# Kernel tuning notes

Measured on AMD Instinct MI355X. Metric: run time of the kernel, lower is better.

## Reference

```python
import jax, jax.numpy as jnp
import numpy as np


def fps(xyz, npoint):
    # Farthest point sampling. xyz: [B, N, 3] -> idx [B, npoint] int32
    B, N, _ = xyz.shape
    d0 = jnp.full((B, N), 1e10, xyz.dtype)
    far0 = jnp.zeros((B,), jnp.int32)

    def step(carry, _):
        dist, far = carry
        centroid = jnp.take_along_axis(xyz, far[:, None, None], axis=1)  # [B,1,3]
        d = jnp.sum((xyz - centroid) ** 2, axis=-1)                      # [B,N]
        dist = jnp.minimum(dist, d)
        nxt = jnp.argmax(dist, axis=-1).astype(jnp.int32)
        return (dist, nxt), far

    _, idx = jax.lax.scan(step, (d0, far0), None, length=npoint)
    return idx.T  # [B, npoint]


def ball_query(radius, nsample, xyz, new_xyz):
    # xyz [B,N,3], new_xyz [B,S,3] -> idx [B,S,nsample] int32
    N = xyz.shape[1]
    sqr = (jnp.sum(new_xyz ** 2, -1)[:, :, None]
           + jnp.sum(xyz ** 2, -1)[:, None, :]
           - 2.0 * jnp.einsum('bsd,bnd->bsn', new_xyz, xyz))  # [B,S,N]
    idx = jnp.broadcast_to(jnp.arange(N, dtype=jnp.int32), sqr.shape)
    idx = jnp.where(sqr > radius * radius, N, idx)
    idx = jnp.sort(idx, axis=-1)[..., :nsample]
    first = idx[..., :1]  # centers are in xyz, so at least one in-radius index exists
    return jnp.where(idx == N, first, idx)


def _gather(x, idx):
    # x [B,N,C], idx [B,S,K] -> [B,S,K,C]
    return jax.vmap(lambda xb, ib: xb[ib])(x, idx)


def set_abstraction(xyz, points, npoint, radius, nsample, layers):
    # xyz [B,N,3]; points [B,N,D] or None; layers: list of (W [Co,Ci], b [Co])
    fps_idx = fps(xyz, npoint)                                   # [B,S]
    new_xyz = jnp.take_along_axis(xyz, fps_idx[..., None], axis=1)  # [B,S,3]
    idx = ball_query(radius, nsample, xyz, new_xyz)              # [B,S,K]
    grouped = _gather(xyz, idx) - new_xyz[:, :, None, :]         # [B,S,K,3] centered
    if points is not None:
        grouped = jnp.concatenate([grouped, _gather(points, idx)], axis=-1)
    feats = grouped  # [B,S,K,Cin]
    for W, b in layers:  # shared 1x1 conv MLP (BN folded, eval mode) + ReLU
        feats = jax.nn.relu(jnp.einsum('bskc,oc->bsko', feats, W) + b)
    new_points = jnp.max(feats, axis=2)  # max-pool over neighborhood -> [B,S,Cout]
    return new_xyz, new_points.transpose(0, 2, 1)  # [B,S,3], [B,Cout,S]


def setup_inputs() -> dict:
    key = jax.random.key(0)
    ks = jax.random.split(key, 13)
    xyz = jax.random.uniform(ks[0], (8, 6, 32768), dtype=jnp.float32)
    dims1 = [(64, 6), (64, 64), (128, 64)]
    dims2 = [(128, 131), (128, 128), (285, 128)]
    inp = {'xyz': xyz}
    i = 1
    for pre, dims in (('sa1', dims1), ('sa2', dims2)):
        for j, (o, c) in enumerate(dims, 1):
            inp[f'{pre}_w{j}'] = jax.random.normal(ks[i], (o, c), jnp.float32) * (1.0 / np.sqrt(c))
            inp[f'{pre}_b{j}'] = jax.random.normal(ks[i + 6], (o,), jnp.float32) * 0.05
            i += 1
    return inp


def reference(xyz, sa1_w1, sa1_b1, sa1_w2, sa1_b2, sa1_w3, sa1_b3,
              sa2_w1, sa2_b1, sa2_w2, sa2_b2, sa2_w3, sa2_b3):
    norm = xyz[:, 3:, :].transpose(0, 2, 1)   # [B,N,3]
    xyz3 = xyz[:, :3, :].transpose(0, 2, 1)   # [B,N,3]
    l1_xyz, l1_points = set_abstraction(
        xyz3, norm, 512, 0.025, 32,
        [(sa1_w1, sa1_b1), (sa1_w2, sa1_b2), (sa1_w3, sa1_b3)])
    l2_xyz, l2_points = set_abstraction(
        l1_xyz, l1_points.transpose(0, 2, 1), 256, 0.05, 64,
        [(sa2_w1, sa2_b1), (sa2_w2, sa2_b2), (sa2_w3, sa2_b3)])
    return l2_xyz.transpose(0, 2, 1), l2_points.transpose(0, 2, 1)  # [B,3,256],[B,256,285]
```

## Files before the change

kernel.cpp:

```cpp
#include <hip/hip_runtime.h>

#define N1 32768
#define NP1 512
#define NS1 32
#define N2 512
#define NP2 256
#define NS2 64

__device__ __forceinline__ float fadd(float a, float b){ return __fadd_rn(a,b); }
__device__ __forceinline__ float fmul(float a, float b){ return __fmul_rn(a,b); }
__device__ __forceinline__ float fsub(float a, float b){ return __fsub_rn(a,b); }

__device__ __forceinline__ float dist3(float px,float py,float pz,float cx,float cy,float cz){
    float dx = fsub(px,cx), dy = fsub(py,cy), dz = fsub(pz,cz);
    return fadd(fadd(fmul(dx,dx), fmul(dy,dy)), fmul(dz,dz));
}
__device__ __forceinline__ float sumsq3(float x,float y,float z){
    return fadd(fadd(fmul(x,x), fmul(y,y)), fmul(z,z));
}
__device__ __forceinline__ float dot3(float ax,float ay,float az,float bx,float by,float bz){
    return fadd(fadd(fmul(ax,bx), fmul(ay,by)), fmul(az,bz));
}

__device__ __forceinline__ unsigned long long shflmax64(unsigned long long k, int off){
    unsigned long long o = __shfl_xor(k, off, 64);
    return o > k ? o : k;
}

#define FPS1_M  16
#define FPS1_TB 256

__global__ __launch_bounds__(FPS1_TB) void fps1_kernel(const float* __restrict__ xyz,
                                                       float* __restrict__ new_xyz1,
                                                       unsigned long long* __restrict__ bests)
{
    const int m = blockIdx.x;
    const int b = blockIdx.y;
    const int t = threadIdx.x;
    const int lane = t & 63;
    const int wid  = t >> 6;
    const int slot = m*4 + wid;
    const float* xb = xyz + (size_t)b * 6 * N1;

    const int base = m * (N1 / FPS1_M);
    float px[8], py[8], pz[8], dd[8];
#pragma unroll
    for (int j = 0; j < 8; ++j) {
        int n = base + t + j * FPS1_TB;
        px[j] = xb[n];
        py[j] = xb[N1 + n];
        pz[j] = xb[2*N1 + n];
        dd[j] = 1e10f;
    }

    float cx = xb[0], cy = xb[N1], cz = xb[2*N1];

    for (int s = 0; s < NP1; ++s) {
        if (m == 0 && t == 0) {
            float* o = new_xyz1 + ((size_t)b*NP1 + s)*3;
            o[0] = cx; o[1] = cy; o[2] = cz;
        }
        if (s == NP1 - 1) break;

        float bv = -1.0f; int bi = base + t;
#pragma unroll
        for (int j = 0; j < 8; ++j) {
            float d  = dist3(px[j],py[j],pz[j],cx,cy,cz);
            float nd = fminf(dd[j], d);
            dd[j] = nd;
            if (nd > bv) { bv = nd; bi = base + t + j*FPS1_TB; }
        }
        unsigned long long pk = ((unsigned long long)__float_as_uint(bv) << 15)
                              | (unsigned long long)(32767 - bi);
        pk = shflmax64(pk, 1);  pk = shflmax64(pk, 2);  pk = shflmax64(pk, 4);
        pk = shflmax64(pk, 8);  pk = shflmax64(pk, 16); pk = shflmax64(pk, 32);

        unsigned long long* slotPar = bests + ((size_t)b*2 + (s & 1))*64;
        if (lane == 0)
            __hip_atomic_store(slotPar + slot, (pk << 10) | (unsigned long long)s,
                               __ATOMIC_RELAXED, __HIP_MEMORY_SCOPE_AGENT);

        unsigned long long myv = 0; bool done = false;
        float ccx = 0.f, ccy = 0.f, ccz = 0.f;
        while (__ballot(done) != 0xFFFFFFFFFFFFFFFFull) {
            if (!done) {
                unsigned long long v = __hip_atomic_load(slotPar + lane,
                                         __ATOMIC_RELAXED, __HIP_MEMORY_SCOPE_AGENT);
                if ((unsigned)(v & 1023ull) == (unsigned)s) {
                    done = true; myv = v;
                    int idx = 32767 - (int)((v >> 10) & 0x7fffull);
                    ccx = xb[idx]; ccy = xb[N1 + idx]; ccz = xb[2*N1 + idx];
                }
            }
        }
        unsigned long long w = myv;
        w = shflmax64(w, 1);  w = shflmax64(w, 2);  w = shflmax64(w, 4);
        w = shflmax64(w, 8);  w = shflmax64(w, 16); w = shflmax64(w, 32);
        int wl = (int)__ffsll(__ballot(myv == w)) - 1;
        cx = __shfl(ccx, wl, 64);
        cy = __shfl(ccy, wl, 64);
        cz = __shfl(ccz, wl, 64);
    }
}

__global__ __launch_bounds__(64) void fps2_kernel(const float* __restrict__ new_xyz1,
                                                  float* __restrict__ new_xyz2,
                                                  float* __restrict__ out0)
{
    const int b = blockIdx.x;
    const int t = threadIdx.x;
    __shared__ float c3[N2*3];
    const float* src = new_xyz1 + (size_t)b*N2*3;
    for (int e = t; e < N2*3; e += 64) c3[e] = src[e];
    __syncthreads();

    float px[8], py[8], pz[8], dd[8];
#pragma unroll
    for (int j = 0; j < 8; ++j) {
        int n = t + j*64;
        px[j] = c3[n*3]; py[j] = c3[n*3+1]; pz[j] = c3[n*3+2];
        dd[j] = 1e10f;
    }
    int cur = 0;
    for (int s = 0; s < NP2; ++s) {
        float cx = c3[cur*3], cy = c3[cur*3+1], cz = c3[cur*3+2];
        if (t == 0) {
            float* o = new_xyz2 + ((size_t)b*NP2 + s)*3;
            o[0]=cx; o[1]=cy; o[2]=cz;
            out0[b*3*NP2 + s]         = cx;
            out0[b*3*NP2 + NP2 + s]   = cy;
            out0[b*3*NP2 + 2*NP2 + s] = cz;
        }
        float bv = -1.0f; int bi = 0;
#pragma unroll
        for (int j = 0; j < 8; ++j) {
            float d  = dist3(px[j],py[j],pz[j],cx,cy,cz);
            float nd = fminf(dd[j], d);
            dd[j] = nd;
            int n = t + j*64;
            if (nd > bv) { bv = nd; bi = n; }
        }
        unsigned long long pk = ((unsigned long long)__float_as_uint(bv) << 9)
                              | (unsigned long long)(511 - bi);
        pk = shflmax64(pk, 1);  pk = shflmax64(pk, 2);  pk = shflmax64(pk, 4);
        pk = shflmax64(pk, 8);  pk = shflmax64(pk, 16); pk = shflmax64(pk, 32);
        cur = 511 - (int)(pk & 511ull);
    }
}

__global__ __launch_bounds__(64) void ball1_kernel(const float* __restrict__ xyz,
                                                   const float* __restrict__ new_xyz1,
                                                   int* __restrict__ idx1, float r2)
{
    const int s = blockIdx.x, b = blockIdx.y;
    const int lane = threadIdx.x;
    const float* xb = xyz + (size_t)b*6*N1;
    const float* cp = new_xyz1 + ((size_t)b*NP1 + s)*3;
    float cx = cp[0], cy = cp[1], cz = cp[2];
    float snew = sumsq3(cx,cy,cz);
    int* out = idx1 + ((size_t)b*NP1 + s)*NS1;
    int cnt = 0, first = 0;
    for (int ch = 0; ch < N1/64; ++ch) {
        int n = ch*64 + lane;
        float x = xb[n], y = xb[N1+n], z = xb[2*N1+n];
        float sx  = sumsq3(x,y,z);
        float dt  = dot3(cx,cy,cz,x,y,z);
        float sqr = fsub(fadd(snew, sx), fmul(2.0f, dt));
        bool inb = !(sqr > r2);
        unsigned long long mask = __ballot(inb);
        if (mask) {
            if (cnt == 0) first = ch*64 + (int)(__ffsll((unsigned long long)mask) - 1);
            if (inb) {
                int pos = cnt + (int)__popcll(mask & ((1ull << lane) - 1ull));
                if (pos < NS1) out[pos] = n;
            }
            cnt += (int)__popcll(mask);
            if (cnt >= NS1) break;
        }
    }
    int c = cnt < NS1 ? cnt : NS1;
    if (lane < NS1 && lane >= c) out[lane] = first;
}

__global__ __launch_bounds__(64) void ball2_kernel(const float* __restrict__ new_xyz1,
                                                   const float* __restrict__ new_xyz2,
                                                   int* __restrict__ idx2, float r2)
{
    const int s = blockIdx.x, b = blockIdx.y;
    const int lane = threadIdx.x;
    const float* pb = new_xyz1 + (size_t)b*N2*3;
    const float* cp = new_xyz2 + ((size_t)b*NP2 + s)*3;
    float cx = cp[0], cy = cp[1], cz = cp[2];
    float snew = sumsq3(cx,cy,cz);
    int* out = idx2 + ((size_t)b*NP2 + s)*NS2;
    int cnt = 0, first = 0;
    for (int ch = 0; ch < N2/64; ++ch) {
        int n = ch*64 + lane;
        float x = pb[n*3], y = pb[n*3+1], z = pb[n*3+2];
        float sx  = sumsq3(x,y,z);
        float dt  = dot3(cx,cy,cz,x,y,z);
        float sqr = fsub(fadd(snew, sx), fmul(2.0f, dt));
        bool inb = !(sqr > r2);
        unsigned long long mask = __ballot(inb);
        if (mask) {
            if (cnt == 0) first = ch*64 + (int)(__ffsll((unsigned long long)mask) - 1);
            if (inb) {
                int pos = cnt + (int)__popcll(mask & ((1ull << lane) - 1ull));
                if (pos < NS2) out[pos] = n;
            }
            cnt += (int)__popcll(mask);
            if (cnt >= NS2) break;
        }
    }
    int c = cnt < NS2 ? cnt : NS2;
    if (lane >= c) out[lane] = first;
}

__global__ __launch_bounds__(256) void mlp1_kernel(const float* __restrict__ xyz,
    const float* __restrict__ new_xyz1, const int* __restrict__ idx1,
    const float* __restrict__ W1, const float* __restrict__ B1,
    const float* __restrict__ W2, const float* __restrict__ B2,
    const float* __restrict__ W3, const float* __restrict__ B3,
    float* __restrict__ l1_points)
{
    const int s = blockIdx.x, b = blockIdx.y;
    const int t = threadIdx.x;
    const float* xb = xyz + (size_t)b*6*N1;
    __shared__ __align__(16) float inb_[NS1][6];
    __shared__ __align__(16) float h1_[NS1][64];
    __shared__ __align__(16) float h2_[NS1][64];
    __shared__ __align__(16) float red_[2][128];
    __shared__ int sidx[NS1];

    const float* cp = new_xyz1 + ((size_t)b*NP1 + s)*3;
    float c0 = cp[0], c1 = cp[1], c2 = cp[2];
    if (t < NS1) sidx[t] = idx1[((size_t)b*NP1+s)*NS1 + t];
    __syncthreads();
    if (t < NS1*6) {
        int k = t / 6, c = t % 6;
        int n = sidx[k];
        float v = xb[(size_t)c*N1 + n];
        if (c == 0) v -= c0; else if (c == 1) v -= c1; else if (c == 2) v -= c2;
        inb_[k][c] = v;
    }
    __syncthreads();
    {
        int o = t & 63, kg = t >> 6;
        float w[6];
#pragma unroll
        for (int c = 0; c < 6; ++c) w[c] = W1[o*6+c];
        float bias = B1[o];
#pragma unroll
        for (int kk = 0; kk < 8; ++kk) {
            int k = kg*8 + kk;
            float a = 0.f;
#pragma unroll
            for (int c = 0; c < 6; ++c) a = fmaf(inb_[k][c], w[c], a);
            h1_[k][o] = fmaxf(a + bias, 0.f);
        }
    }
    __syncthreads();
    {
        int o = t & 63, kg = t >> 6;
        float acc[8] = {};
        for (int ch = 0; ch < 8; ++ch) {
            const float4 wa = *(const float4*)&W2[o*64 + ch*8];
            const float4 wbv = *(const float4*)&W2[o*64 + ch*8 + 4];
#pragma unroll
            for (int kk = 0; kk < 8; ++kk) {
                int k = kg*8+kk;
                const float4 a0 = *(const float4*)&h1_[k][ch*8];
                const float4 a1 = *(const float4*)&h1_[k][ch*8+4];
                acc[kk] = fmaf(a0.x, wa.x, acc[kk]);
                acc[kk] = fmaf(a0.y, wa.y, acc[kk]);
                acc[kk] = fmaf(a0.z, wa.z, acc[kk]);
                acc[kk] = fmaf(a0.w, wa.w, acc[kk]);
                acc[kk] = fmaf(a1.x, wbv.x, acc[kk]);
                acc[kk] = fmaf(a1.y, wbv.y, acc[kk]);
                acc[kk] = fmaf(a1.z, wbv.z, acc[kk]);
                acc[kk] = fmaf(a1.w, wbv.w, acc[kk]);
            }
        }
        float bias = B2[o];
#pragma unroll
        for (int kk = 0; kk < 8; ++kk) h2_[kg*8+kk][o] = fmaxf(acc[kk] + bias, 0.f);
    }
    __syncthreads();
    {
        int o = t & 127, kg = t >> 7;
        float acc[16] = {};
        for (int ch = 0; ch < 8; ++ch) {
            const float4 wa = *(const float4*)&W3[o*64 + ch*8];
            const float4 wbv = *(const float4*)&W3[o*64 + ch*8 + 4];
#pragma unroll
            for (int kk = 0; kk < 16; ++kk) {
                int k = kg*16+kk;
                const float4 a0 = *(const float4*)&h2_[k][ch*8];
                const float4 a1 = *(const float4*)&h2_[k][ch*8+4];
                acc[kk] = fmaf(a0.x, wa.x, acc[kk]);
                acc[kk] = fmaf(a0.y, wa.y, acc[kk]);
                acc[kk] = fmaf(a0.z, wa.z, acc[kk]);
                acc[kk] = fmaf(a0.w, wa.w, acc[kk]);
                acc[kk] = fmaf(a1.x, wbv.x, acc[kk]);
                acc[kk] = fmaf(a1.y, wbv.y, acc[kk]);
                acc[kk] = fmaf(a1.z, wbv.z, acc[kk]);
                acc[kk] = fmaf(a1.w, wbv.w, acc[kk]);
            }
        }
        float bias = B3[o];
        float m = -1e30f;
#pragma unroll
        for (int kk = 0; kk < 16; ++kk) m = fmaxf(m, fmaxf(acc[kk] + bias, 0.f));
        red_[kg][o] = m;
    }
    __syncthreads();
    if (t < 128) {
        float m = fmaxf(red_[0][t], red_[1][t]);
        l1_points[((size_t)b*NP1+s)*128 + t] = m;
    }
}

__global__ __launch_bounds__(256) void mlp2_kernel(
    const float* __restrict__ new_xyz1, const float* __restrict__ l1_points,
    const float* __restrict__ new_xyz2, const int* __restrict__ idx2,
    const float* __restrict__ W1, const float* __restrict__ B1,
    const float* __restrict__ W2, const float* __restrict__ B2,
    const float* __restrict__ W3, const float* __restrict__ B3,
    float* __restrict__ out1)
{
    const int s = blockIdx.x, b = blockIdx.y;
    const int t = threadIdx.x;
    __shared__ __align__(16) float inb_[32][132];
    __shared__ __align__(16) float h1_[32][128];
    __shared__ __align__(16) float h2_[32][128];
    __shared__ int sidx[NS2];

    const float* cp = new_xyz2 + ((size_t)b*NP2+s)*3;
    float c0=cp[0], c1=cp[1], c2=cp[2];
    if (t < NS2) sidx[t] = idx2[((size_t)b*NP2+s)*NS2 + t];

    const int o1 = t & 63, o2 = o1 + 64, g = t >> 6;
    float vmax0 = -1e30f, vmax1 = -1e30f;

    for (int half = 0; half < 2; ++half) {
        __syncthreads();
        for (int e = t; e < 32*32; e += 256) {
            int kk = e >> 5, c4 = e & 31;
            int n = sidx[half*32 + kk];
            *(float4*)&inb_[kk][c4*4] =
                *(const float4*)&l1_points[((size_t)b*N2 + n)*128 + c4*4];
        }
        for (int e = t; e < 32*3; e += 256) {
            int kk = e / 3, c = e % 3;
            int n = sidx[half*32 + kk];
            inb_[kk][128 + c] = new_xyz1[((size_t)b*N2 + n)*3 + c]
                              - (c==0 ? c0 : (c==1 ? c1 : c2));
        }
        __syncthreads();
        {
            float accA[8] = {}, accB[8] = {};
            for (int ch = 0; ch < 16; ++ch) {
                float wa[8], wbv[8];
#pragma unroll
                for (int j = 0; j < 8; ++j) {
                    wa[j]  = W1[o1*131 + 3 + ch*8 + j];
                    wbv[j] = W1[o2*131 + 3 + ch*8 + j];
                }
#pragma unroll
                for (int kk = 0; kk < 8; ++kk) {
                    int k = g*8 + kk;
                    const float4 a0 = *(const float4*)&inb_[k][ch*8];
                    const float4 a1 = *(const float4*)&inb_[k][ch*8+4];
                    accA[kk] = fmaf(a0.x, wa[0], accA[kk]);
                    accA[kk] = fmaf(a0.y, wa[1], accA[kk]);
                    accA[kk] = fmaf(a0.z, wa[2], accA[kk]);
                    accA[kk] = fmaf(a0.w, wa[3], accA[kk]);
                    accA[kk] = fmaf(a1.x, wa[4], accA[kk]);
                    accA[kk] = fmaf(a1.y, wa[5], accA[kk]);
                    accA[kk] = fmaf(a1.z, wa[6], accA[kk]);
                    accA[kk] = fmaf(a1.w, wa[7], accA[kk]);
                    accB[kk] = fmaf(a0.x, wbv[0], accB[kk]);
                    accB[kk] = fmaf(a0.y, wbv[1], accB[kk]);
                    accB[kk] = fmaf(a0.z, wbv[2], accB[kk]);
                    accB[kk] = fmaf(a0.w, wbv[3], accB[kk]);
                    accB[kk] = fmaf(a1.x, wbv[4], accB[kk]);
                    accB[kk] = fmaf(a1.y, wbv[5], accB[kk]);
                    accB[kk] = fmaf(a1.z, wbv[6], accB[kk]);
                    accB[kk] = fmaf(a1.w, wbv[7], accB[kk]);
                }
            }
            float ta0=W1[o1*131+0], ta1=W1[o1*131+1], ta2=W1[o1*131+2];
            float tb0=W1[o2*131+0], tb1=W1[o2*131+1], tb2=W1[o2*131+2];
            float biasA = B1[o1], biasB = B1[o2];
#pragma unroll
            for (int kk = 0; kk < 8; ++kk) {
                int k = g*8 + kk;
                float f0 = inb_[k][128], f1 = inb_[k][129], f2 = inb_[k][130];
                float vA = accA[kk];
                vA = fmaf(f0, ta0, vA); vA = fmaf(f1, ta1, vA); vA = fmaf(f2, ta2, vA);
                float vB = accB[kk];
                vB = fmaf(f0, tb0, vB); vB = fmaf(f1, tb1, vB); vB = fmaf(f2, tb2, vB);
                h1_[k][o1] = fmaxf(vA + biasA, 0.f);
                h1_[k][o2] = fmaxf(vB + biasB, 0.f);
            }
        }
        __syncthreads();
        {
            float accA[8] = {}, accB[8] = {};
            for (int ch = 0; ch < 16; ++ch) {
                const float4 wa0 = *(const float4*)&W2[o1*128 + ch*8];
                const float4 wa1 = *(const float4*)&W2[o1*128 + ch*8 + 4];
                const float4 wb0 = *(const float4*)&W2[o2*128 + ch*8];
                const float4 wb1 = *(const float4*)&W2[o2*128 + ch*8 + 4];
#pragma unroll
                for (int kk = 0; kk < 8; ++kk) {
                    int k = g*8 + kk;
                    const float4 a0 = *(const float4*)&h1_[k][ch*8];
                    const float4 a1 = *(const float4*)&h1_[k][ch*8+4];
                    accA[kk] = fmaf(a0.x, wa0.x, accA[kk]);
                    accA[kk] = fmaf(a0.y, wa0.y, accA[kk]);
                    accA[kk] = fmaf(a0.z, wa0.z, accA[kk]);
                    accA[kk] = fmaf(a0.w, wa0.w, accA[kk]);
                    accA[kk] = fmaf(a1.x, wa1.x, accA[kk]);
                    accA[kk] = fmaf(a1.y, wa1.y, accA[kk]);
                    accA[kk] = fmaf(a1.z, wa1.z, accA[kk]);
                    accA[kk] = fmaf(a1.w, wa1.w, accA[kk]);
                    accB[kk] = fmaf(a0.x, wb0.x, accB[kk]);
                    accB[kk] = fmaf(a0.y, wb0.y, accB[kk]);
                    accB[kk] = fmaf(a0.z, wb0.z, accB[kk]);
                    accB[kk] = fmaf(a0.w, wb0.w, accB[kk]);
                    accB[kk] = fmaf(a1.x, wb1.x, accB[kk]);
                    accB[kk] = fmaf(a1.y, wb1.y, accB[kk]);
                    accB[kk] = fmaf(a1.z, wb1.z, accB[kk]);
                    accB[kk] = fmaf(a1.w, wb1.w, accB[kk]);
                }
            }
            float biasA = B2[o1], biasB = B2[o2];
#pragma unroll
            for (int kk = 0; kk < 8; ++kk) {
                int k = g*8 + kk;
                h2_[k][o1] = fmaxf(accA[kk] + biasA, 0.f);
                h2_[k][o2] = fmaxf(accB[kk] + biasB, 0.f);
            }
        }
        __syncthreads();
        {
            {
                float acc[32] = {};
                for (int ch = 0; ch < 16; ++ch) {
                    const float4 w0 = *(const float4*)&W3[t*128 + ch*8];
                    const float4 w1 = *(const float4*)&W3[t*128 + ch*8 + 4];
#pragma unroll
                    for (int kk = 0; kk < 32; ++kk) {
                        const float4 a0 = *(const float4*)&h2_[kk][ch*8];
                        const float4 a1 = *(const float4*)&h2_[kk][ch*8+4];
                        acc[kk] = fmaf(a0.x, w0.x, acc[kk]);
                        acc[kk] = fmaf(a0.y, w0.y, acc[kk]);
                        acc[kk] = fmaf(a0.z, w0.z, acc[kk]);
                        acc[kk] = fmaf(a0.w, w0.w, acc[kk]);
                        acc[kk] = fmaf(a1.x, w1.x, acc[kk]);
                        acc[kk] = fmaf(a1.y, w1.y, acc[kk]);
                        acc[kk] = fmaf(a1.z, w1.z, acc[kk]);
                        acc[kk] = fmaf(a1.w, w1.w, acc[kk]);
                    }
                }
                float bias = B3[t];
                float mm = vmax0;
#pragma unroll
                for (int kk = 0; kk < 32; ++kk) mm = fmaxf(mm, fmaxf(acc[kk] + bias, 0.f));
                vmax0 = mm;
            }
            if (t < 29) {
                int o = t + 256;
                float acc[32] = {};
                for (int ch = 0; ch < 16; ++ch) {
                    const float4 w0 = *(const float4*)&W3[o*128 + ch*8];
                    const float4 w1 = *(const float4*)&W3[o*128 + ch*8 + 4];
#pragma unroll
                    for (int kk = 0; kk < 32; ++kk) {
                        const float4 a0 = *(const float4*)&h2_[kk][ch*8];
                        const float4 a1 = *(const float4*)&h2_[kk][ch*8+4];
                        acc[kk] = fmaf(a0.x, w0.x, acc[kk]);
                        acc[kk] = fmaf(a0.y, w0.y, acc[kk]);
                        acc[kk] = fmaf(a0.z, w0.z, acc[kk]);
                        acc[kk] = fmaf(a0.w, w0.w, acc[kk]);
                        acc[kk] = fmaf(a1.x, w1.x, acc[kk]);
                        acc[kk] = fmaf(a1.y, w1.y, acc[kk]);
                        acc[kk] = fmaf(a1.z, w1.z, acc[kk]);
                        acc[kk] = fmaf(a1.w, w1.w, acc[kk]);
                    }
                }
                float bias = B3[o];
                float mm = vmax1;
#pragma unroll
                for (int kk = 0; kk < 32; ++kk) mm = fmaxf(mm, fmaxf(acc[kk] + bias, 0.f));
                vmax1 = mm;
            }
        }
    }
    out1[((size_t)b*NP2+s)*285 + t] = vmax0;
    if (t < 29) out1[((size_t)b*NP2+s)*285 + t + 256] = vmax1;
}

extern "C" void kernel_launch(void* const* d_in, const int* in_sizes, int n_in,
                              void* d_out, int out_size, void* d_ws, size_t ws_size,
                              hipStream_t stream)
{
    (void)in_sizes; (void)n_in; (void)out_size; (void)ws_size;
    const float* xyz  = (const float*)d_in[0];
    const float* s1w1 = (const float*)d_in[1];  const float* s1b1 = (const float*)d_in[2];
    const float* s1w2 = (const float*)d_in[3];  const float* s1b2 = (const float*)d_in[4];
    const float* s1w3 = (const float*)d_in[5];  const float* s1b3 = (const float*)d_in[6];
    const float* s2w1 = (const float*)d_in[7];  const float* s2b1 = (const float*)d_in[8];
    const float* s2w2 = (const float*)d_in[9];  const float* s2b2 = (const float*)d_in[10];
    const float* s2w3 = (const float*)d_in[11]; const float* s2b3 = (const float*)d_in[12];

    float* ws        = (float*)d_ws;
    float* new_xyz1  = ws;
    float* new_xyz2  = ws + 12288;
    float* l1_points = ws + 18432;
    int*   idx1      = (int*)(ws + 542720);
    int*   idx2      = idx1 + 131072;
    unsigned long long* bests = (unsigned long long*)(ws + 804864);

    float* out0 = (float*)d_out;
    float* out1 = out0 + 8*3*256;

    const float r2a = (float)(0.025*0.025);
    const float r2b = (float)(0.05*0.05);

    fps1_kernel <<<dim3(FPS1_M, 8), dim3(FPS1_TB), 0, stream>>>(xyz, new_xyz1, bests);
    ball1_kernel<<<dim3(NP1, 8),    dim3(64),      0, stream>>>(xyz, new_xyz1, idx1, r2a);
    mlp1_kernel <<<dim3(NP1, 8),    dim3(256),     0, stream>>>(xyz, new_xyz1, idx1,
                    s1w1,s1b1,s1w2,s1b2,s1w3,s1b3, l1_points);
    fps2_kernel <<<dim3(8),         dim3(64),      0, stream>>>(new_xyz1, new_xyz2, out0);
    ball2_kernel<<<dim3(NP2, 8),    dim3(64),      0, stream>>>(new_xyz1, new_xyz2, idx2, r2b);
    mlp2_kernel <<<dim3(NP2, 8),    dim3(256),     0, stream>>>(new_xyz1, l1_points, new_xyz2, idx2,
                    s2w1,s2b1,s2w2,s2b2,s2w3,s2b3, out1);
}
```

Before: 1.876 ms.

## Reduce FPS1 grid-sync slots per block and co-schedule independent kernels

In the first farthest-point-sampling kernel, the four waves of each block now reduce through shared memory with a __syncthreads, so each block publishes one global slot instead of four. Each spinning wave then polls only 16 slots instead of 64, shrinking the per-step cross-block exchange. Separately, fps2 is folded into the ball1 launch as an extra block, and ball2 is folded into the mlp1 launch as extra blocks, to overlap independent work and drop two launches. The trade-off is an added block barrier per FPS step and heterogeneous blocks inside the merged kernels, including 256-thread blocks where only one wave does the ball2 work.

Result: slower. 2.156 ms (+15.0%).

```diff
diff --git a/kernel.cpp b/kernel.cpp
--- a/kernel.cpp
+++ b/kernel.cpp
@@ -39,8 +39,9 @@
     const int t = threadIdx.x;
     const int lane = t & 63;
     const int wid  = t >> 6;
-    const int slot = m*4 + wid;
     const float* xb = xyz + (size_t)b * 6 * N1;
+
+    __shared__ unsigned long long wbuf[2][4];
 
     const int base = m * (N1 / FPS1_M);
     float px[8], py[8], pz[8], dd[8];
@@ -74,13 +75,18 @@
                               | (unsigned long long)(32767 - bi);
         pk = shflmax64(pk, 1);  pk = shflmax64(pk, 2);  pk = shflmax64(pk, 4);
         pk = shflmax64(pk, 8);  pk = shflmax64(pk, 16); pk = shflmax64(pk, 32);
-
-        unsigned long long* slotPar = bests + ((size_t)b*2 + (s & 1))*64;
-        if (lane == 0)
-            __hip_atomic_store(slotPar + slot, (pk << 10) | (unsigned long long)s,
-                               __ATOMIC_RELAXED, __HIP_MEMORY_SCOPE_AGENT);
-
-        unsigned long long myv = 0; bool done = false;
+        if (lane == 0) wbuf[s & 1][wid] = pk;
+        __syncthreads();
+
+        unsigned long long* slotPar = bests + ((size_t)b*2 + (s & 1))*FPS1_M;
+        if (wid == 0) {
+            unsigned long long k4 = (lane < 4) ? wbuf[s & 1][lane] : 0ull;
+            k4 = shflmax64(k4, 1); k4 = shflmax64(k4, 2);
+            if (lane == 0)
+                __hip_atomic_store(slotPar + m, (k4 << 10) | (unsigned long long)s,
+                                   __ATOMIC_RELAXED, __HIP_MEMORY_SCOPE_AGENT);
+        }
+        unsigned long long myv = 0; bool done = (lane >= FPS1_M);
         float ccx = 0.f, ccy = 0.f, ccz = 0.f;
         while (__ballot(done) != 0xFFFFFFFFFFFFFFFFull) {
             if (!done) {
@@ -103,128 +109,131 @@
     }
 }
 
-__global__ __launch_bounds__(64) void fps2_kernel(const float* __restrict__ new_xyz1,
-                                                  float* __restrict__ new_xyz2,
-                                                  float* __restrict__ out0)
+__global__ __launch_bounds__(64) void ball1_fps2_kernel(const float* __restrict__ xyz,
+                                                        const float* __restrict__ new_xyz1,
+                                                        int* __restrict__ idx1, float r2,
+                                                        float* __restrict__ new_xyz2,
+                                                        float* __restrict__ out0)
 {
-    const int b = blockIdx.x;
-    const int t = threadIdx.x;
-    __shared__ float c3[N2*3];
-    const float* src = new_xyz1 + (size_t)b*N2*3;
-    for (int e = t; e < N2*3; e += 64) c3[e] = src[e];
-    __syncthreads();
-
-    float px[8], py[8], pz[8], dd[8];
-#pragma unroll
-    for (int j = 0; j < 8; ++j) {
-        int n = t + j*64;
-        px[j] = c3[n*3]; py[j] = c3[n*3+1]; pz[j] = c3[n*3+2];
-        dd[j] = 1e10f;
-    }
-    int cur = 0;
-    for (int s = 0; s < NP2; ++s) {
-        float cx = c3[cur*3], cy = c3[cur*3+1], cz = c3[cur*3+2];
-        if (t == 0) {
-            float* o = new_xyz2 + ((size_t)b*NP2 + s)*3;
-            o[0]=cx; o[1]=cy; o[2]=cz;
-            out0[b*3*NP2 + s]         = cx;
-            out0[b*3*NP2 + NP2 + s]   = cy;
-            out0[b*3*NP2 + 2*NP2 + s] = cz;
-        }
-        float bv = -1.0f; int bi = 0;
+    const int b = blockIdx.y;
+    const int lane = threadIdx.x;
+
+    if (blockIdx.x < NP1) {
+        const int s = blockIdx.x;
+        const float* xb = xyz + (size_t)b*6*N1;
+        const float* cp = new_xyz1 + ((size_t)b*NP1 + s)*3;
+        float cx = cp[0], cy = cp[1], cz = cp[2];
+        float snew = sumsq3(cx,cy,cz);
+        int* out = idx1 + ((size_t)b*NP1 + s)*NS1;
+        int cnt = 0, first = 0;
+        for (int ch = 0; ch < N1/64; ++ch) {
+            int n = ch*64 + lane;
+            float x = xb[n], y = xb[N1+n], z = xb[2*N1+n];
+            float sx  = sumsq3(x,y,z);
+            float dt  = dot3(cx,cy,cz,x,y,z);
+            float sqr = fsub(fadd(snew, sx), fmul(2.0f, dt));
+            bool inb = !(sqr > r2);
+            unsigned long long mask = __ballot(inb);
+            if (mask) {
+                if (cnt == 0) first = ch*64 + (int)(__ffsll((unsigned long long)mask) - 1);
+                if (inb) {
+                    int pos = cnt + (int)__popcll(mask & ((1ull << lane) - 1ull));
+                    if (pos < NS1) out[pos] = n;
+                }
+                cnt += (int)__popcll(mask);
+                if (cnt >= NS1) break;
+            }
+        }
+        int c = cnt < NS1 ? cnt : NS1;
+        if (lane < NS1 && lane >= c) out[lane] = first;
+    } else {
+        __shared__ float c3[N2*3];
+        const int t = lane;
+        const float* src = new_xyz1 + (size_t)b*N2*3;
+        for (int e = t; e < N2*3; e += 64) c3[e] = src[e];
+        __syncthreads();
+
+        float px[8], py[8], pz[8], dd[8];
 #pragma unroll
         for (int j = 0; j < 8; ++j) {
-            float d  = dist3(px[j],py[j],pz[j],cx,cy,cz);
-            float nd = fminf(dd[j], d);
-            dd[j] = nd;
             int n = t + j*64;
-            if (nd > bv) { bv = nd; bi = n; }
-        }
-        unsigned long long pk = ((unsigned long long)__float_as_uint(bv) << 9)
-                              | (unsigned long long)(511 - bi);
-        pk = shflmax64(pk, 1);  pk = shflmax64(pk, 2);  pk = shflmax64(pk, 4);
-        pk = shflmax64(pk, 8);  pk = shflmax64(pk, 16); pk = shflmax64(pk, 32);
-        cur = 511 - (int)(pk & 511ull);
-    }
-}
-
-__global__ __launch_bounds__(64) void ball1_kernel(const float* __restrict__ xyz,
-                                                   const float* __restrict__ new_xyz1,
-                                                   int* __restrict__ idx1, float r2)
-{
-    const int s = blockIdx.x, b = blockIdx.y;
-    const int lane = threadIdx.x;
-    const float* xb = xyz + (size_t)b*6*N1;
-    const float* cp = new_xyz1 + ((size_t)b*NP1 + s)*3;
-    float cx = cp[0], cy = cp[1], cz = cp[2];
-    float snew = sumsq3(cx,cy,cz);
-    int* out = idx1 + ((size_t)b*NP1 + s)*NS1;
-    int cnt = 0, first = 0;
-    for (int ch = 0; ch < N1/64; ++ch) {
-        int n = ch*64 + lane;
-        float x = xb[n], y = xb[N1+n], z = xb[2*N1+n];
-        float sx  = sumsq3(x,y,z);
-        float dt  = dot3(cx,cy,cz,x,y,z);
-        float sqr = fsub(fadd(snew, sx), fmul(2.0f, dt));
-        bool inb = !(sqr > r2);
-        unsigned long long mask = __ballot(inb);
-        if (mask) {
-            if (cnt == 0) first = ch*64 + (int)(__ffsll((unsigned long long)mask) - 1);
-            if (inb) {
-                int pos = cnt + (int)__popcll(mask & ((1ull << lane) - 1ull));
-                if (pos < NS1) out[pos] = n;
-            }
-            cnt += (int)__popcll(mask);
-            if (cnt >= NS1) break;
-        }
-    }
-    int c = cnt < NS1 ? cnt : NS1;
-    if (lane < NS1 && lane >= c) out[lane] = first;
-}
-
-__global__ __launch_bounds__(64) void ball2_kernel(const float* __restrict__ new_xyz1,
-                                                   const float* __restrict__ new_xyz2,
-                                                   int* __restrict__ idx2, float r2)
-{
-    const int s = blockIdx.x, b = blockIdx.y;
-    const int lane = threadIdx.x;
-    const float* pb = new_xyz1 + (size_t)b*N2*3;
-    const float* cp = new_xyz2 + ((size_t)b*NP2 + s)*3;
-    float cx = cp[0], cy = cp[1], cz = cp[2];
-    float snew = sumsq3(cx,cy,cz);
-    int* out = idx2 + ((size_t)b*NP2 + s)*NS2;
-    int cnt = 0, first = 0;
-    for (int ch = 0; ch < N2/64; ++ch) {
-        int n = ch*64 + lane;
-        float x = pb[n*3], y = pb[n*3+1], z = pb[n*3+2];
-        float sx  = sumsq3(x,y,z);
-        float dt  = dot3(cx,cy,cz,x,y,z);
-        float sqr = fsub(fadd(snew, sx), fmul(2.0f, dt));
-        bool inb = !(sqr > r2);
-        unsigned long long mask = __ballot(inb);
-        if (mask) {
-            if (cnt == 0) first = ch*64 + (int)(__ffsll((unsigned long long)mask) - 1);
-            if (inb) {
-                int pos = cnt + (int)__popcll(mask & ((1ull << lane) - 1ull));
-                if (pos < NS2) out[pos] = n;
-            }
-            cnt += (int)__popcll(mask);
-            if (cnt >= NS2) break;
-        }
-    }
-    int c = cnt < NS2 ? cnt : NS2;
-    if (lane >= c) out[lane] = first;
-}
-
-__global__ __launch_bounds__(256) void mlp1_kernel(const float* __restrict__ xyz,
+            px[j] = c3[n*3]; py[j] = c3[n*3+1]; pz[j] = c3[n*3+2];
+            dd[j] = 1e10f;
+        }
+        int cur = 0;
+        for (int s = 0; s < NP2; ++s) {
+            float cx = c3[cur*3], cy = c3[cur*3+1], cz = c3[cur*3+2];
+            if (t == 0) {
+                float* o = new_xyz2 + ((size_t)b*NP2 + s)*3;
+                o[0]=cx; o[1]=cy; o[2]=cz;
+                out0[b*3*NP2 + s]         = cx;
+                out0[b*3*NP2 + NP2 + s]   = cy;
+                out0[b*3*NP2 + 2*NP2 + s] = cz;
+            }
+            float bv = -1.0f; int bi = 0;
+#pragma unroll
+            for (int j = 0; j < 8; ++j) {
+                float d  = dist3(px[j],py[j],pz[j],cx,cy,cz);
+                float nd = fminf(dd[j], d);
+                dd[j] = nd;
+                int n = t + j*64;
+                if (nd > bv) { bv = nd; bi = n; }
+            }
+            unsigned long long pk = ((unsigned long long)__float_as_uint(bv) << 9)
+                                  | (unsigned long long)(511 - bi);
+            pk = shflmax64(pk, 1);  pk = shflmax64(pk, 2);  pk = shflmax64(pk, 4);
+            pk = shflmax64(pk, 8);  pk = shflmax64(pk, 16); pk = shflmax64(pk, 32);
+            cur = 511 - (int)(pk & 511ull);
+        }
+    }
+}
+
+__global__ __launch_bounds__(256) void mlp1_ball2_kernel(const float* __restrict__ xyz,
     const float* __restrict__ new_xyz1, const int* __restrict__ idx1,
     const float* __restrict__ W1, const float* __restrict__ B1,
     const float* __restrict__ W2, const float* __restrict__ B2,
     const float* __restrict__ W3, const float* __restrict__ B3,
-    float* __restrict__ l1_points)
+    float* __restrict__ l1_points,
+    const float* __restrict__ new_xyz2, int* __restrict__ idx2, float r2b)
 {
-    const int s = blockIdx.x, b = blockIdx.y;
+    const int b = blockIdx.y;
     const int t = threadIdx.x;
+
+    if (blockIdx.x >= NP1) {
+        if (t < 64) {
+            const int s = blockIdx.x - NP1;
+            const int lane = t;
+            const float* pb = new_xyz1 + (size_t)b*N2*3;
+            const float* cp = new_xyz2 + ((size_t)b*NP2 + s)*3;
+            float cx = cp[0], cy = cp[1], cz = cp[2];
+            float snew = sumsq3(cx,cy,cz);
+            int* out = idx2 + ((size_t)b*NP2 + s)*NS2;
+            int cnt = 0, first = 0;
+            for (int ch = 0; ch < N2/64; ++ch) {
+                int n = ch*64 + lane;
+                float x = pb[n*3], y = pb[n*3+1], z = pb[n*3+2];
+                float sx  = sumsq3(x,y,z);
+                float dt  = dot3(cx,cy,cz,x,y,z);
+                float sqr = fsub(fadd(snew, sx), fmul(2.0f, dt));
+                bool inb = !(sqr > r2b);
+                unsigned long long mask = __ballot(inb);
+                if (mask) {
+                    if (cnt == 0) first = ch*64 + (int)(__ffsll((unsigned long long)mask) - 1);
+                    if (inb) {
+                        int pos = cnt + (int)__popcll(mask & ((1ull << lane) - 1ull));
+                        if (pos < NS2) out[pos] = n;
+                    }
+                    cnt += (int)__popcll(mask);
+                    if (cnt >= NS2) break;
+                }
+            }
+            int c = cnt < NS2 ? cnt : NS2;
+            if (lane >= c) out[lane] = first;
+        }
+        return;
+    }
+
+    const int s = blockIdx.x;
     const float* xb = xyz + (size_t)b*6*N1;
     __shared__ __align__(16) float inb_[NS1][6];
     __shared__ __align__(16) float h1_[NS1][64];
@@ -529,12 +538,12 @@
     const float r2a = (float)(0.025*0.025);
     const float r2b = (float)(0.05*0.05);
 
-    fps1_kernel <<<dim3(FPS1_M, 8), dim3(FPS1_TB), 0, stream>>>(xyz, new_xyz1, bests);
-    ball1_kernel<<<dim3(NP1, 8),    dim3(64),      0, stream>>>(xyz, new_xyz1, idx1, r2a);
-    mlp1_kernel <<<dim3(NP1, 8),    dim3(256),     0, stream>>>(xyz, new_xyz1, idx1,
-                    s1w1,s1b1,s1w2,s1b2,s1w3,s1b3, l1_points);
-    fps2_kernel <<<dim3(8),         dim3(64),      0, stream>>>(new_xyz1, new_xyz2, out0);
-    ball2_kernel<<<dim3(NP2, 8),    dim3(64),      0, stream>>>(new_xyz1, new_xyz2, idx2, r2b);
-    mlp2_kernel <<<dim3(NP2, 8),    dim3(256),     0, stream>>>(new_xyz1, l1_points, new_xyz2, idx2,
-                    s2w1,s2b1,s2w2,s2b2,s2w3,s2b3, out1);
-}
+    fps1_kernel      <<<dim3(FPS1_M, 8),    dim3(FPS1_TB), 0, stream>>>(xyz, new_xyz1, bests);
+    ball1_fps2_kernel<<<dim3(NP1+1, 8),     dim3(64),      0, stream>>>(xyz, new_xyz1, idx1, r2a,
+                         new_xyz2, out0);
+    mlp1_ball2_kernel<<<dim3(NP1+NP2, 8),   dim3(256),     0, stream>>>(xyz, new_xyz1, idx1,
+                         s1w1,s1b1,s1w2,s1b2,s1w3,s1b3, l1_points,
+                         new_xyz2, idx2, r2b);
+    mlp2_kernel      <<<dim3(NP2, 8),       dim3(256),     0, stream>>>(new_xyz1, l1_points,
+                         new_xyz2, idx2, s2w1,s2b1,s2w2,s2b2,s2w3,s2b3, out1);
+}
```
